# Kernel tuning notes

Measured on AMD Instinct MI355X. Metric: run time of the kernel, lower is better.

## Reference

```python
import jax, jax.numpy as jnp
import numpy as np

BLOCK = 8           # block_size
FREQ_REMOVE = 2     # freq_remove_num


def _ceil16(n: int) -> int:
    # replicate DCT.padding: four rounds of ceil-div-2, then *16
    for _ in range(4):
        n = (n + 1) // 2
    return 16 * n


def _dct_mat(N: int) -> jnp.ndarray:
    # orthonormal DCT-II matrix D s.t. (D @ v) == scipy.fftpack.dct(v, norm='ortho')
    n = jnp.arange(N, dtype=jnp.float32)
    k = n[:, None]
    D = jnp.cos(jnp.pi * (2.0 * n[None, :] + 1.0) * k / (2.0 * N))
    scale = jnp.where(jnp.arange(N) == 0, jnp.sqrt(1.0 / N), jnp.sqrt(2.0 / N)).astype(jnp.float32)
    return D * scale[:, None]


def setup_inputs() -> dict:
    key = jax.random.key(0)
    x = jax.random.uniform(key, (1, 4096, 4096), dtype=jnp.float32)  # image in [0,1)
    return {"x": x}


def reference(x) -> jnp.ndarray:
    _, h, w = x.shape
    H, W = _ceil16(h), _ceil16(w)
    h1 = (H - h) // 2
    w1 = (W - w) // 2
    x = jnp.pad(x, ((0, 0), (h1, H - h - h1), (w1, W - w - w1)))
    # (x*255).byte(): truncation; inputs in [0,1) -> floor, no uint8 wrap
    x = jnp.floor(x * 255.0)
    Hb, Wb = H // BLOCK, W // BLOCK
    # [1,H,W] -> [Hb, Wb, b, b] (drop leading singleton like iterating .numpy())
    blk = x.reshape(Hb, BLOCK, Wb, BLOCK).transpose(0, 2, 1, 3)
    # Faithful to source: dct along axis=1 (Wb block-index axis) then axis=2 (block row axis)
    Dw = _dct_mat(Wb)      # [Wb, Wb]
    Db = _dct_mat(BLOCK)   # [b, b]
    y = jnp.einsum('kw,hwij->hkij', Dw, blk)   # DCT over block-column index
    y = jnp.einsum('mi,hkij->hkmj', Db, y)     # DCT over intra-block rows
    # retain_high_freq: zero first FREQ_REMOVE rows and cols of each bxb block
    mask = jnp.ones((BLOCK, BLOCK), y.dtype).at[:FREQ_REMOVE, :].set(0.0).at[:, :FREQ_REMOVE].set(0.0)
    y = y * mask  # broadcast over [Hb, Wb, b, b]
    # permute back and flatten to [1, H, W]
    out = y.transpose(0, 2, 1, 3).reshape(1, H, W)
    return out
```

## Files before the change

### kernel.cpp

```cpp
#include <hip/hip_runtime.h>
#include <math.h>

#define ZSLAB 98304
#define DSLAB 16384

typedef __attribute__((ext_vector_type(8))) __bf16 bf16x8;
typedef __attribute__((ext_vector_type(4))) float  f32x4;

__device__ __forceinline__ unsigned short f2bf(float f) {
  union { float f; unsigned u; } v; v.f = f;
  unsigned r = v.u + 0x7fffu + ((v.u >> 16) & 1u);
  return (unsigned short)(r >> 16);
}
__device__ __forceinline__ float bf2f(unsigned short s) {
  union { unsigned u; float f; } v; v.u = ((unsigned)s) << 16;
  return v.f;
}

__device__ const float DBC[8][8] = {
  { 0.35355339f,  0.35355339f,  0.35355339f,  0.35355339f,  0.35355339f,  0.35355339f,  0.35355339f,  0.35355339f},
  { 0.49039264f,  0.41573481f,  0.27778512f,  0.09754516f, -0.09754516f, -0.27778512f, -0.41573481f, -0.49039264f},
  { 0.46193977f,  0.19134172f, -0.19134172f, -0.46193977f, -0.46193977f, -0.19134172f,  0.19134172f,  0.46193977f},
  { 0.41573481f, -0.09754516f, -0.49039264f, -0.27778512f,  0.27778512f,  0.49039264f,  0.09754516f, -0.41573481f},
  { 0.35355339f, -0.35355339f, -0.35355339f,  0.35355339f,  0.35355339f, -0.35355339f, -0.35355339f,  0.35355339f},
  { 0.27778512f, -0.49039264f,  0.09754516f,  0.41573481f, -0.41573481f, -0.09754516f,  0.49039264f, -0.27778512f},
  { 0.19134172f, -0.46193977f,  0.46193977f, -0.19134172f, -0.19134172f,  0.46193977f, -0.46193977f,  0.19134172f},
  { 0.09754516f, -0.27778512f,  0.41573481f, -0.49039264f,  0.49039264f, -0.41573481f,  0.27778512f, -0.09754516f}
};

__global__ __launch_bounds__(256) void pack_all(const float* __restrict__ x,
                                                unsigned short* __restrict__ zc,
                                                unsigned short* __restrict__ dwf) {
  const int h = blockIdx.x, t = threadIdx.x;

  {
    const int idx = (blockIdx.y * 512 + blockIdx.x) * 256 + t;
    const int k = idx >> 9, w = idx & 511;
    const int n = (k * (2 * w + 1)) & 2047;
    const float c = __cosf((float)n * 0.0030679615757712823f);
    const float scale = (k == 0) ? 0.04419417382415922f : 0.0625f;
    const int kko = w >> 5, g = (w >> 3) & 3, e = w & 7, s = (k >> 1) & 3;
    dwf[(size_t)kko * DSLAB + k * 32 + ((g ^ s) << 3) + e] = f2bf(c * scale);
  }

  const int c0 = blockIdx.y * 2048 + t * 8;
  const float* xb = x + (size_t)(h * 8) * 4096 + c0;
  float q[8][8];
#pragma unroll
  for (int i = 0; i < 8; ++i) {
    float4 a = *reinterpret_cast<const float4*>(xb + (size_t)i * 4096);
    float4 b = *reinterpret_cast<const float4*>(xb + (size_t)i * 4096 + 4);
    q[i][0] = floorf(a.x * 255.0f); q[i][1] = floorf(a.y * 255.0f);
    q[i][2] = floorf(a.z * 255.0f); q[i][3] = floorf(a.w * 255.0f);
    q[i][4] = floorf(b.x * 255.0f); q[i][5] = floorf(b.y * 255.0f);
    q[i][6] = floorf(b.z * 255.0f); q[i][7] = floorf(b.w * 255.0f);
  }
  const int w0 = c0 >> 3;
  const int kko = w0 >> 5, g = (w0 >> 3) & 3, e = w0 & 7;
#pragma unroll
  for (int m = 2; m < 8; ++m) {
    const int row = h * 6 + (m - 2);
    const int s = (row >> 1) & 3;
    const size_t base = (size_t)row * 32 + ((g ^ s) << 3) + e;
#pragma unroll
    for (int j = 2; j < 8; ++j) {
      float v = 0.0f;
#pragma unroll
      for (int i = 0; i < 8; ++i) v = fmaf(DBC[m][i], q[i][j], v);
      zc[(size_t)((j - 2) * 16 + kko) * ZSLAB + base] = f2bf(v);
    }
  }
}

__device__ __forceinline__ void gload16(const unsigned short* g, unsigned short* l) {
  __builtin_amdgcn_global_load_lds(
      (__attribute__((address_space(1))) void*)(g),
      (__attribute__((address_space(3))) void*)(l),
      16, 0, 0);
}

__global__ __launch_bounds__(384, 6) void fused_dct(const unsigned short* __restrict__ zc,
                                                    const unsigned short* __restrict__ dwf,
                                                    float* __restrict__ out) {
  const int bid = blockIdx.x;
  const int mt  = bid & 63;
  const int nt  = bid >> 6;

  __shared__ __align__(16) unsigned char SM[40960];
  unsigned short* Obuf = (unsigned short*)SM;

  const int tid  = threadIdx.x;
  const int lane = tid & 63;
  const int wv   = tid >> 6;
  const int l15  = lane & 15;
  const int hlf  = (tid >= 192) ? 1 : 0;
  const int rem  = tid - hlf * 192;

  f32x4 acc[3][2] = {};

#define STAGE(buf, kkos)                                                             \
  do {                                                                               \
    unsigned short* As_ = (unsigned short*)(SM + (buf) * 20480);                     \
    _Pragma("unroll")                                                                \
    for (int q_ = 0; q_ < 3; ++q_) {                                                 \
      const int j2_ = 2 * q_ + hlf;                                                  \
      gload16(zc + (size_t)(j2_ * 16 + (kkos)) * ZSLAB + mt * 1536 + rem * 8,        \
              As_ + (q_ * 384 + tid) * 8);                                           \
    }                                                                                \
    if (tid < 128)                                                                   \
      gload16(dwf + (size_t)(kkos) * DSLAB + nt * 1024 + tid * 8,                    \
              (unsigned short*)(SM + 18432 + (buf) * 20480) + tid * 8);              \
  } while (0)

  STAGE(0, 0);
  __syncthreads();
  for (int t = 0; t < 16; ++t) {
    const int cur = t & 1;
    if (t < 15) STAGE(cur ^ 1, t + 1);
    const unsigned short* Ap = (const unsigned short*)(SM + cur * 20480) + wv * 1536;
    const unsigned short* Bp = (const unsigned short*)(SM + 18432 + cur * 20480);
    bf16x8 bfr[2];
#pragma unroll
    for (int nf = 0; nf < 2; ++nf) {
      const int r = nf * 16 + l15;
      bfr[nf] = *reinterpret_cast<const bf16x8*>(
          Bp + r * 32 + (((lane >> 4) ^ ((r >> 1) & 3)) << 3));
    }
#pragma unroll
    for (int mf = 0; mf < 3; ++mf) {
      const int r = mf * 16 + l15;
      const bf16x8 afr = *reinterpret_cast<const bf16x8*>(
          Ap + r * 32 + (((lane >> 4) ^ ((r >> 1) & 3)) << 3));
      acc[mf][0] = __builtin_amdgcn_mfma_f32_16x16x32_bf16(afr, bfr[0], acc[mf][0], 0, 0, 0);
      acc[mf][1] = __builtin_amdgcn_mfma_f32_16x16x32_bf16(afr, bfr[1], acc[mf][1], 0, 0, 0);
    }
    __syncthreads();
  }
#undef STAGE

  unsigned short* Ob = Obuf + wv * 1632;
#pragma unroll
  for (int mf = 0; mf < 3; ++mf)
#pragma unroll
    for (int nf = 0; nf < 2; ++nf)
#pragma unroll
      for (int p = 0; p < 4; ++p)
        Ob[(mf * 16 + (lane >> 4) * 4 + p) * 34 + nf * 16 + l15] = f2bf(acc[mf][nf][p]);
  __syncthreads();

  float* outb = out + (size_t)(mt * 64) * 4096 + nt * 256;
  for (int v = tid; v < 4096; v += 384) {
    const int row64 = v >> 6;
    const int c4 = (v & 63) << 2;
    f32x4 val = {0.0f, 0.0f, 0.0f, 0.0f};
    const int m = row64 & 7;
    if (m >= 2) {
      const int row48 = (row64 >> 3) * 6 + (m - 2);
      const int kk = c4 >> 3, jb = c4 & 4;
#pragma unroll
      for (int e = 0; e < 4; ++e) {
        const int j = jb + e;
        if (j >= 2)
          val[e] = bf2f(Obuf[(j - 2) * 1632 + row48 * 34 + kk]);
      }
    }
    *reinterpret_cast<f32x4*>(outb + (size_t)row64 * 4096 + c4) = val;
  }
}

extern "C" void kernel_launch(void* const* d_in, const int* in_sizes, int n_in,
                              void* d_out, int out_size, void* d_ws, size_t ws_size,
                              hipStream_t stream) {
  const float* x = (const float*)d_in[0];
  float* out = (float*)d_out;
  char* ws = (char*)d_ws;

  unsigned short* dwf = (unsigned short*)ws;
  unsigned short* zc  = (unsigned short*)(ws + 524288);

  pack_all<<<dim3(512, 2), 256, 0, stream>>>(x, zc, dwf);
  fused_dct<<<1024, 384, 0, stream>>>(zc, dwf, out);
}
```

Before: 49.65 us.

## Keep two K-stages in flight with partial vmcnt waits instead of syncthreads

Restructures the double-buffered main loop so two stages are prefetched up front. Each iteration waits only for the older stage's loads (vmcnt(4)) with raw s_barrier, and issues the next load into the freed buffer after compute, so global-to-LDS loads overlap more with the MFMAs. The B-tile load becomes unconditional, with all threads duplicating the 128-thread copy, which keeps the per-thread vmcnt count uniform. This relies on correct hand-written waitcnt accounting; a miscount could race on LDS.

Result: faster. 46.85 us (-5.6%).

```diff
diff --git a/kernel.cpp b/kernel.cpp
--- a/kernel.cpp
+++ b/kernel.cpp
@@ -107,36 +107,47 @@
       gload16(zc + (size_t)(j2_ * 16 + (kkos)) * ZSLAB + mt * 1536 + rem * 8,        \
               As_ + (q_ * 384 + tid) * 8);                                           \
     }                                                                                \
-    if (tid < 128)                                                                   \
-      gload16(dwf + (size_t)(kkos) * DSLAB + nt * 1024 + tid * 8,                    \
-              (unsigned short*)(SM + 18432 + (buf) * 20480) + tid * 8);              \
+    gload16(dwf + (size_t)(kkos) * DSLAB + nt * 1024 + (tid & 127) * 8,              \
+            (unsigned short*)(SM + 18432 + (buf) * 20480) + (tid & 127) * 8);        \
+  } while (0)
+
+#define COMPUTE(cur)                                                                 \
+  do {                                                                               \
+    const unsigned short* Ap = (const unsigned short*)(SM + (cur) * 20480) + wv * 1536; \
+    const unsigned short* Bp = (const unsigned short*)(SM + 18432 + (cur) * 20480);  \
+    bf16x8 bfr[2];                                                                   \
+    _Pragma("unroll")                                                                \
+    for (int nf = 0; nf < 2; ++nf) {                                                 \
+      const int r_ = nf * 16 + l15;                                                  \
+      bfr[nf] = *reinterpret_cast<const bf16x8*>(                                    \
+          Bp + r_ * 32 + (((lane >> 4) ^ ((r_ >> 1) & 3)) << 3));                    \
+    }                                                                                \
+    _Pragma("unroll")                                                                \
+    for (int mf = 0; mf < 3; ++mf) {                                                 \
+      const int r_ = mf * 16 + l15;                                                  \
+      const bf16x8 afr = *reinterpret_cast<const bf16x8*>(                           \
+          Ap + r_ * 32 + (((lane >> 4) ^ ((r_ >> 1) & 3)) << 3));                    \
+      acc[mf][0] = __builtin_amdgcn_mfma_f32_16x16x32_bf16(afr, bfr[0], acc[mf][0], 0, 0, 0); \
+      acc[mf][1] = __builtin_amdgcn_mfma_f32_16x16x32_bf16(afr, bfr[1], acc[mf][1], 0, 0, 0); \
+    }                                                                                \
   } while (0)
 
   STAGE(0, 0);
-  __syncthreads();
-  for (int t = 0; t < 16; ++t) {
+  STAGE(1, 1);
+  for (int t = 0; t < 15; ++t) {
     const int cur = t & 1;
-    if (t < 15) STAGE(cur ^ 1, t + 1);
-    const unsigned short* Ap = (const unsigned short*)(SM + cur * 20480) + wv * 1536;
-    const unsigned short* Bp = (const unsigned short*)(SM + 18432 + cur * 20480);
-    bf16x8 bfr[2];
-#pragma unroll
-    for (int nf = 0; nf < 2; ++nf) {
-      const int r = nf * 16 + l15;
-      bfr[nf] = *reinterpret_cast<const bf16x8*>(
-          Bp + r * 32 + (((lane >> 4) ^ ((r >> 1) & 3)) << 3));
-    }
-#pragma unroll
-    for (int mf = 0; mf < 3; ++mf) {
-      const int r = mf * 16 + l15;
-      const bf16x8 afr = *reinterpret_cast<const bf16x8*>(
-          Ap + r * 32 + (((lane >> 4) ^ ((r >> 1) & 3)) << 3));
-      acc[mf][0] = __builtin_amdgcn_mfma_f32_16x16x32_bf16(afr, bfr[0], acc[mf][0], 0, 0, 0);
-      acc[mf][1] = __builtin_amdgcn_mfma_f32_16x16x32_bf16(afr, bfr[1], acc[mf][1], 0, 0, 0);
-    }
-    __syncthreads();
+    asm volatile("s_waitcnt vmcnt(4)" ::: "memory");
+    __builtin_amdgcn_s_barrier();
+    COMPUTE(cur);
+    asm volatile("s_waitcnt lgkmcnt(0)" ::: "memory");
+    __builtin_amdgcn_s_barrier();
+    if (t < 14) STAGE(cur, t + 2);
   }
+  asm volatile("s_waitcnt vmcnt(0)" ::: "memory");
+  __builtin_amdgcn_s_barrier();
+  COMPUTE(1);
 #undef STAGE
+#undef COMPUTE
 
   unsigned short* Ob = Obuf + wv * 1632;
 #pragma unroll
```

## Preload full B slab to LDS and use per-wave A double buffering without barriers

Applied to the files above, without the earlier changes.

The DCT-weight (B) tiles for all 16 k-steps are loaded into shared memory once up front. Each wave then streams only its own A slab through a private double buffer and waits on manual vmcnt/lgkmcnt counters instead of a block-wide __syncthreads every k-step. The aim is to remove the per-iteration barrier and redundant B staging so loads overlap better with MFMA. In exchange LDS use rises to about 68KB and occupancy drops (launch bounds go from 6 to 3). Correctness now depends on the hand-counted waitcnt values.

Measured after the change: 52.45 us. +5.7%, slower.

```diff
diff --git a/kernel.cpp b/kernel.cpp
--- a/kernel.cpp
+++ b/kernel.cpp
@@ -79,64 +79,74 @@
       16, 0, 0);
 }
 
-__global__ __launch_bounds__(384, 6) void fused_dct(const unsigned short* __restrict__ zc,
+__global__ __launch_bounds__(384, 3) void fused_dct(const unsigned short* __restrict__ zc,
                                                     const unsigned short* __restrict__ dwf,
                                                     float* __restrict__ out) {
   const int bid = blockIdx.x;
   const int mt  = bid & 63;
   const int nt  = bid >> 6;
 
-  __shared__ __align__(16) unsigned char SM[40960];
+  __shared__ __align__(16) unsigned char SM[69632];
+  unsigned short* Bsh  = (unsigned short*)SM;
   unsigned short* Obuf = (unsigned short*)SM;
 
   const int tid  = threadIdx.x;
   const int lane = tid & 63;
   const int wv   = tid >> 6;
   const int l15  = lane & 15;
-  const int hlf  = (tid >= 192) ? 1 : 0;
-  const int rem  = tid - hlf * 192;
+
+  const unsigned short* Asrc = zc + (size_t)(wv * 16) * ZSLAB + (size_t)mt * 1536;
+  unsigned short* Abuf = (unsigned short*)(SM + 32768 + wv * 6144);
 
   f32x4 acc[3][2] = {};
 
-#define STAGE(buf, kkos)                                                             \
+  for (int c = wv; c < 16; c += 6) {
+#pragma unroll
+    for (int hf = 0; hf < 2; ++hf)
+      gload16(dwf + (size_t)c * DSLAB + nt * 1024 + hf * 512 + lane * 8,
+              Bsh + c * 1024 + hf * 512 + lane * 8);
+  }
+  __syncthreads();
+
+#define STAGE_A(buf, kko)                                                            \
   do {                                                                               \
-    unsigned short* As_ = (unsigned short*)(SM + (buf) * 20480);                     \
     _Pragma("unroll")                                                                \
-    for (int q_ = 0; q_ < 3; ++q_) {                                                 \
-      const int j2_ = 2 * q_ + hlf;                                                  \
-      gload16(zc + (size_t)(j2_ * 16 + (kkos)) * ZSLAB + mt * 1536 + rem * 8,        \
-              As_ + (q_ * 384 + tid) * 8);                                           \
-    }                                                                                \
-    if (tid < 128)                                                                   \
-      gload16(dwf + (size_t)(kkos) * DSLAB + nt * 1024 + tid * 8,                    \
-              (unsigned short*)(SM + 18432 + (buf) * 20480) + tid * 8);              \
+    for (int q_ = 0; q_ < 3; ++q_)                                                   \
+      gload16(Asrc + (size_t)(kko) * ZSLAB + q_ * 512 + lane * 8,                    \
+              Abuf + (buf) * 1536 + q_ * 512 + lane * 8);                            \
   } while (0)
 
-  STAGE(0, 0);
-  __syncthreads();
+  STAGE_A(0, 0);
+  STAGE_A(1, 1);
+#pragma unroll
   for (int t = 0; t < 16; ++t) {
-    const int cur = t & 1;
-    if (t < 15) STAGE(cur ^ 1, t + 1);
-    const unsigned short* Ap = (const unsigned short*)(SM + cur * 20480) + wv * 1536;
-    const unsigned short* Bp = (const unsigned short*)(SM + 18432 + cur * 20480);
+    if (t < 15) { asm volatile("s_waitcnt vmcnt(3)" ::: "memory"); }
+    else        { asm volatile("s_waitcnt vmcnt(0)" ::: "memory"); }
+    const unsigned short* Ap = Abuf + (t & 1) * 1536;
+    const unsigned short* Bp = Bsh + t * 1024;
     bf16x8 bfr[2];
 #pragma unroll
     for (int nf = 0; nf < 2; ++nf) {
-      const int r = nf * 16 + l15;
+      const int r_ = nf * 16 + l15;
       bfr[nf] = *reinterpret_cast<const bf16x8*>(
-          Bp + r * 32 + (((lane >> 4) ^ ((r >> 1) & 3)) << 3));
+          Bp + r_ * 32 + (((lane >> 4) ^ ((r_ >> 1) & 3)) << 3));
     }
 #pragma unroll
     for (int mf = 0; mf < 3; ++mf) {
-      const int r = mf * 16 + l15;
+      const int r_ = mf * 16 + l15;
       const bf16x8 afr = *reinterpret_cast<const bf16x8*>(
-          Ap + r * 32 + (((lane >> 4) ^ ((r >> 1) & 3)) << 3));
+          Ap + r_ * 32 + (((lane >> 4) ^ ((r_ >> 1) & 3)) << 3));
       acc[mf][0] = __builtin_amdgcn_mfma_f32_16x16x32_bf16(afr, bfr[0], acc[mf][0], 0, 0, 0);
       acc[mf][1] = __builtin_amdgcn_mfma_f32_16x16x32_bf16(afr, bfr[1], acc[mf][1], 0, 0, 0);
     }
-    __syncthreads();
+    if (t < 14) {
+      asm volatile("s_waitcnt lgkmcnt(0)" ::: "memory");
+      STAGE_A(t & 1, t + 2);
+    }
   }
-#undef STAGE
+#undef STAGE_A
+
+  __syncthreads();
 
   unsigned short* Ob = Obuf + wv * 1632;
 #pragma unroll
```

## Load A fragments directly to registers and preload all B tiles in LDS

Applied to the files above, without the earlier changes.

Drops the double-buffered LDS staging of the A operand. Each wave now reads its MFMA A fragments straight from global memory into registers with inline-asm dwordx4 loads, double-buffered across two register sets and ordered with explicit vmcnt waits. All 16 K-slices of the DCT matrix B are loaded into LDS once at the start, and the per-iteration __syncthreads are removed. The pack kernel stops applying the XOR swizzle to zc so the direct global reads stay contiguous. This trades LDS traffic and barriers for more register pressure and more uncoalesced global-load latency that the waves must hide.

New measurement: 49.66 us. No clear change (+0.0%).

```diff
diff --git a/kernel.cpp b/kernel.cpp
--- a/kernel.cpp
+++ b/kernel.cpp
@@ -56,12 +56,11 @@
     q[i][6] = floorf(b.z * 255.0f); q[i][7] = floorf(b.w * 255.0f);
   }
   const int w0 = c0 >> 3;
-  const int kko = w0 >> 5, g = (w0 >> 3) & 3, e = w0 & 7;
+  const int kko = w0 >> 5, w31 = w0 & 31;
 #pragma unroll
   for (int m = 2; m < 8; ++m) {
     const int row = h * 6 + (m - 2);
-    const int s = (row >> 1) & 3;
-    const size_t base = (size_t)row * 32 + ((g ^ s) << 3) + e;
+    const size_t base = (size_t)row * 32 + w31;
 #pragma unroll
     for (int j = 2; j < 8; ++j) {
       float v = 0.0f;
@@ -86,57 +85,78 @@
   const int mt  = bid & 63;
   const int nt  = bid >> 6;
 
-  __shared__ __align__(16) unsigned char SM[40960];
+  __shared__ __align__(16) unsigned char SM[32768];
+  unsigned short* Bsh  = (unsigned short*)SM;
   unsigned short* Obuf = (unsigned short*)SM;
 
   const int tid  = threadIdx.x;
   const int lane = tid & 63;
   const int wv   = tid >> 6;
   const int l15  = lane & 15;
-  const int hlf  = (tid >= 192) ? 1 : 0;
-  const int rem  = tid - hlf * 192;
+  const int hi   = lane >> 4;
+
+  for (int c = wv; c < 16; c += 6) {
+#pragma unroll
+    for (int hf = 0; hf < 2; ++hf)
+      gload16(dwf + (size_t)c * DSLAB + nt * 1024 + hf * 512 + lane * 8,
+              Bsh + c * 1024 + hf * 512 + lane * 8);
+  }
+  __syncthreads();
 
   f32x4 acc[3][2] = {};
-
-#define STAGE(buf, kkos)                                                             \
+  const unsigned short* pA0 = zc + (size_t)(wv * 16) * ZSLAB
+                              + (size_t)(mt * 48 + l15) * 32 + hi * 8;
+  const unsigned short* pA1 = pA0 + ZSLAB;
+
+  bf16x8 a0[3], a1[3];
+
+#define ISSUE(dst, p)                                                     \
+  asm volatile("global_load_dwordx4 %0, %3, off\n\t"                     \
+               "global_load_dwordx4 %1, %3, off offset:1024\n\t"         \
+               "global_load_dwordx4 %2, %3, off offset:2048"             \
+               : "=&v"(dst[0]), "=&v"(dst[1]), "=&v"(dst[2])             \
+               : "v"(p)                                                   \
+               : "memory")
+
+#define WAITV(n)                                                          \
+  do {                                                                    \
+    asm volatile("s_waitcnt vmcnt(" #n ")" ::: "memory");                 \
+    __builtin_amdgcn_sched_barrier(0);                                    \
+  } while (0)
+
+#define COMPUTE(AS, t)                                                               \
   do {                                                                               \
-    unsigned short* As_ = (unsigned short*)(SM + (buf) * 20480);                     \
+    const unsigned short* Bp = Bsh + (t) * 1024;                                     \
+    bf16x8 bfr[2];                                                                   \
     _Pragma("unroll")                                                                \
-    for (int q_ = 0; q_ < 3; ++q_) {                                                 \
-      const int j2_ = 2 * q_ + hlf;                                                  \
-      gload16(zc + (size_t)(j2_ * 16 + (kkos)) * ZSLAB + mt * 1536 + rem * 8,        \
-              As_ + (q_ * 384 + tid) * 8);                                           \
+    for (int nf = 0; nf < 2; ++nf) {                                                 \
+      const int r_ = nf * 16 + l15;                                                  \
+      bfr[nf] = *reinterpret_cast<const bf16x8*>(                                    \
+          Bp + r_ * 32 + ((hi ^ ((r_ >> 1) & 3)) << 3));                             \
     }                                                                                \
-    if (tid < 128)                                                                   \
-      gload16(dwf + (size_t)(kkos) * DSLAB + nt * 1024 + tid * 8,                    \
-              (unsigned short*)(SM + 18432 + (buf) * 20480) + tid * 8);              \
+    _Pragma("unroll")                                                                \
+    for (int mf = 0; mf < 3; ++mf) {                                                 \
+      acc[mf][0] = __builtin_amdgcn_mfma_f32_16x16x32_bf16(AS[mf], bfr[0], acc[mf][0], 0, 0, 0); \
+      acc[mf][1] = __builtin_amdgcn_mfma_f32_16x16x32_bf16(AS[mf], bfr[1], acc[mf][1], 0, 0, 0); \
+    }                                                                                \
   } while (0)
 
-  STAGE(0, 0);
+  ISSUE(a0, pA0); pA0 += 2 * ZSLAB;
+  ISSUE(a1, pA1); pA1 += 2 * ZSLAB;
+#pragma unroll
+  for (int tt = 0; tt < 16; tt += 2) {
+    WAITV(3);
+    COMPUTE(a0, tt);
+    if (tt < 14) { ISSUE(a0, pA0); pA0 += 2 * ZSLAB; }
+    if (tt < 14) { WAITV(3); } else { WAITV(0); }
+    COMPUTE(a1, tt + 1);
+    if (tt < 13) { ISSUE(a1, pA1); pA1 += 2 * ZSLAB; }
+  }
+#undef ISSUE
+#undef WAITV
+#undef COMPUTE
+
   __syncthreads();
-  for (int t = 0; t < 16; ++t) {
-    const int cur = t & 1;
-    if (t < 15) STAGE(cur ^ 1, t + 1);
-    const unsigned short* Ap = (const unsigned short*)(SM + cur * 20480) + wv * 1536;
-    const unsigned short* Bp = (const unsigned short*)(SM + 18432 + cur * 20480);
-    bf16x8 bfr[2];
-#pragma unroll
-    for (int nf = 0; nf < 2; ++nf) {
-      const int r = nf * 16 + l15;
-      bfr[nf] = *reinterpret_cast<const bf16x8*>(
-          Bp + r * 32 + (((lane >> 4) ^ ((r >> 1) & 3)) << 3));
-    }
-#pragma unroll
-    for (int mf = 0; mf < 3; ++mf) {
-      const int r = mf * 16 + l15;
-      const bf16x8 afr = *reinterpret_cast<const bf16x8*>(
-          Ap + r * 32 + (((lane >> 4) ^ ((r >> 1) & 3)) << 3));
-      acc[mf][0] = __builtin_amdgcn_mfma_f32_16x16x32_bf16(afr, bfr[0], acc[mf][0], 0, 0, 0);
-      acc[mf][1] = __builtin_amdgcn_mfma_f32_16x16x32_bf16(afr, bfr[1], acc[mf][1], 0, 0, 0);
-    }
-    __syncthreads();
-  }
-#undef STAGE
 
   unsigned short* Ob = Obuf + wv * 1632;
 #pragma unroll
```
